# Kernel tuning notes

Hardware: AMD Instinct MI355X
Metric: run time of the kernel (lower is better)

Reference implementation:

```python
import jax, jax.numpy as jnp
import numpy as np

B, T, D, H, L, V = 4, 1024, 1024, 16, 6, 32000
HS = D // H
FF = 4 * D
EPS = 1e-5


def setup_inputs() -> dict:
    key = jax.random.key(0)
    ks = jax.random.split(key, 16)
    s = 0.02
    n = lambda k, shape: (jax.random.normal(k, shape, jnp.float32) * s)
    return {
        'idx': jax.random.randint(ks[0], (B, T), 0, V),
        'targets': jax.random.randint(ks[1], (B, T), 0, V),
        'tok_emb': n(ks[2], (V, D)),
        'pos_emb': n(ks[3], (T, D)),
        'Wq': n(ks[4], (L, D, H, HS)),
        'Wk': n(ks[5], (L, D, H, HS)),
        'Wv': n(ks[6], (L, D, H, HS)),
        'proj_w': n(ks[7], (L, D, D)),
        'proj_b': jnp.zeros((L, D), jnp.float32),
        'ln1_g': jnp.ones((L, D), jnp.float32),
        'ln1_b': jnp.zeros((L, D), jnp.float32),
        'ln2_g': jnp.ones((L, D), jnp.float32),
        'ln2_b': jnp.zeros((L, D), jnp.float32),
        'ff_w1': n(ks[8], (L, D, FF)),
        'ff_b1': jnp.zeros((L, FF), jnp.float32),
        'ff_w2': n(ks[9], (L, FF, D)),
        'ff_b2': jnp.zeros((L, D), jnp.float32),
        'lnf_g': jnp.ones((D,), jnp.float32),
        'lnf_b': jnp.zeros((D,), jnp.float32),
        'head_w': n(ks[10], (D, V)),
        'head_b': jnp.zeros((V,), jnp.float32),
    }


def _ln(x, g, b):
    m = jnp.mean(x, axis=-1, keepdims=True)
    v = jnp.mean((x - m) ** 2, axis=-1, keepdims=True)
    return (x - m) * jax.lax.rsqrt(v + EPS) * g + b


def _forward(idx, targets, tok_emb, pos_emb, Wq, Wk, Wv, proj_w, proj_b,
             ln1_g, ln1_b, ln2_g, ln2_b, ff_w1, ff_b1, ff_w2, ff_b2,
             lnf_g, lnf_b, head_w, head_b):
    b, t = idx.shape
    x = tok_emb[idx] + pos_emb[:t]                       # [B,T,D]
    mask = jnp.tril(jnp.ones((t, t), bool))              # causal
    scale = jnp.float32(D) ** -0.5                       # NOTE: scales by num_dims (c), as in source
    for l in range(L):
        h = _ln(x, ln1_g[l], ln1_b[l])
        q = jnp.einsum('btd,dhs->bhts', h, Wq[l])        # [B,H,T,HS]
        k = jnp.einsum('btd,dhs->bhts', h, Wk[l])
        v = jnp.einsum('btd,dhs->bhts', h, Wv[l])
        w = jnp.einsum('bhts,bhus->bhtu', q, k) * scale  # [B,H,T,T]
        w = jnp.where(mask, w, -jnp.inf)
        w = jax.nn.softmax(w, axis=-1)
        o = jnp.einsum('bhtu,bhus->bhts', w, v)          # [B,H,T,HS]
        o = o.transpose(0, 2, 1, 3).reshape(b, t, D)     # concat heads
        x = x + jnp.einsum('btd,de->bte', o, proj_w[l]) + proj_b[l]
        h2 = _ln(x, ln2_g[l], ln2_b[l])
        ff = jax.nn.relu(jnp.einsum('btd,df->btf', h2, ff_w1[l]) + ff_b1[l])
        x = x + jnp.einsum('btf,fd->btd', ff, ff_w2[l]) + ff_b2[l]
    x = _ln(x, lnf_g, lnf_b)
    logits = jnp.einsum('btd,dv->btv', x, head_w) + head_b
    logits = logits.reshape(b * t, V)
    tgt = targets.reshape(b * t)
    logp = jax.nn.log_softmax(logits, axis=-1)
    loss = -jnp.mean(jnp.take_along_axis(logp, tgt[:, None], axis=-1))
    return logits, loss


def reference(idx, targets, tok_emb, pos_emb, Wq, Wk, Wv, proj_w, proj_b,
              ln1_g, ln1_b, ln2_g, ln2_b, ff_w1, ff_b1, ff_w2, ff_b2,
              lnf_g, lnf_b, head_w, head_b):
    return _forward(idx, targets, tok_emb, pos_emb, Wq, Wk, Wv, proj_w, proj_b,
                    ln1_g, ln1_b, ln2_g, ln2_b, ff_w1, ff_b1, ff_w2, ff_b2,
                    lnf_g, lnf_b, head_w, head_b)
```

## Files before the change

### kernel.cpp

```cpp
#include <hip/hip_runtime.h>

typedef __attribute__((ext_vector_type(8))) short bf16x8;
typedef __attribute__((ext_vector_type(4))) float f32x4;

#define L_LAYERS 6
#define T_SEQ 1024
#define D_MODEL 1024
#define N_HEAD 16
#define HS 64
#define FF_DIM 4096
#define VOCAB 32000
#define BT_ROWS 4096
#define ATTN_SCALE 0.03125f

__device__ __forceinline__ ushort f2bf(float f) {
  unsigned u = __builtin_bit_cast(unsigned, f);
  unsigned r = (u + 0x7fffu + ((u >> 16) & 1u)) >> 16;
  return (ushort)r;
}
__device__ __forceinline__ float waveRedSum(float v) {
#pragma unroll
  for (int off = 32; off; off >>= 1) v += __shfl_xor(v, off);
  return v;
}
__device__ __forceinline__ void gload16(const void* g, void* l) {
  __builtin_amdgcn_global_load_lds(
      (const __attribute__((address_space(1))) unsigned int*)g,
      (__attribute__((address_space(3))) unsigned int*)l, 16, 0, 0);
}

__global__ __launch_bounds__(256) void embed_kernel(const int* __restrict__ idx,
                                                    const float* __restrict__ tok,
                                                    const float* __restrict__ pos,
                                                    float* __restrict__ x) {
  int row = blockIdx.x;
  int tid = threadIdx.x;
  int t = row & (T_SEQ - 1);
  int id = idx[row];
  float4 tv = ((const float4*)(tok + (size_t)id * D_MODEL))[tid];
  float4 pv = ((const float4*)(pos + (size_t)t * D_MODEL))[tid];
  tv.x += pv.x; tv.y += pv.y; tv.z += pv.z; tv.w += pv.w;
  ((float4*)(x + (size_t)row * D_MODEL))[tid] = tv;
}

__global__ __launch_bounds__(256) void ln_kernel(const float* __restrict__ x,
                                                 const float* __restrict__ g,
                                                 const float* __restrict__ b,
                                                 ushort* __restrict__ out) {
  int row = blockIdx.x;
  int tid = threadIdx.x;
  __shared__ float red[4];
  float4 xv = ((const float4*)(x + (size_t)row * D_MODEL))[tid];
  float s = xv.x + xv.y + xv.z + xv.w;
  s = waveRedSum(s);
  if ((tid & 63) == 0) red[tid >> 6] = s;
  __syncthreads();
  float mean = (red[0] + red[1] + red[2] + red[3]) * (1.0f / D_MODEL);
  __syncthreads();
  float d0 = xv.x - mean, d1 = xv.y - mean, d2 = xv.z - mean, d3 = xv.w - mean;
  float v = d0 * d0 + d1 * d1 + d2 * d2 + d3 * d3;
  v = waveRedSum(v);
  if ((tid & 63) == 0) red[tid >> 6] = v;
  __syncthreads();
  float var = (red[0] + red[1] + red[2] + red[3]) * (1.0f / D_MODEL);
  float rstd = rsqrtf(var + 1e-5f);
  float4 gv = ((const float4*)g)[tid];
  float4 bv = ((const float4*)b)[tid];
  ushort4 o;
  o.x = f2bf(d0 * rstd * gv.x + bv.x);
  o.y = f2bf(d1 * rstd * gv.y + bv.y);
  o.z = f2bf(d2 * rstd * gv.z + bv.z);
  o.w = f2bf(d3 * rstd * gv.w + bv.w);
  ((ushort4*)(out + (size_t)row * D_MODEL))[tid] = o;
}

__device__ __forceinline__ void wconv_body(const float* __restrict__ W,
                                           ushort* __restrict__ WT,
                                           int Kd, int Nd, int n0, int k0) {
  __shared__ ushort tile[64][72];
  int tid = threadIdx.x;
#pragma unroll
  for (int i = 0; i < 4; i++) {
    int c = tid + i * 256;
    int row = c >> 4, cc = c & 15;
    float4 wv = *(const float4*)&W[(size_t)(k0 + row) * Nd + n0 + cc * 4];
    tile[row][cc * 4 + 0] = f2bf(wv.x);
    tile[row][cc * 4 + 1] = f2bf(wv.y);
    tile[row][cc * 4 + 2] = f2bf(wv.z);
    tile[row][cc * 4 + 3] = f2bf(wv.w);
  }
  __syncthreads();
#pragma unroll
  for (int i = 0; i < 2; i++) {
    int c = tid + i * 256;
    int n = c >> 3, kc = c & 7;
    __align__(16) ushort tmp[8];
#pragma unroll
    for (int j = 0; j < 8; j++) tmp[j] = tile[kc * 8 + j][n];
    *(int4*)&WT[(size_t)(n0 + n) * Kd + k0 + kc * 8] = *(const int4*)tmp;
  }
}

__global__ __launch_bounds__(256) void wconv_kernel(const float* __restrict__ W,
                                                    ushort* __restrict__ WT,
                                                    int Kd, int Nd) {
  wconv_body(W, WT, Kd, Nd, blockIdx.x * 64, blockIdx.y * 64);
}

__global__ __launch_bounds__(256) void wconv4_kernel(const float* __restrict__ W0,
                                                     const float* __restrict__ W1,
                                                     const float* __restrict__ W2,
                                                     const float* __restrict__ W3,
                                                     ushort* __restrict__ WT,
                                                     int Kd, int Nd) {
  int z = blockIdx.z;
  const float* W = (z == 0) ? W0 : (z == 1) ? W1 : (z == 2) ? W2 : W3;
  wconv_body(W, WT + (size_t)z * Kd * Nd, Kd, Nd, blockIdx.x * 64, blockIdx.y * 64);
}

__global__ __launch_bounds__(256) void vtrans_kernel(const ushort* __restrict__ v,
                                                     ushort* __restrict__ vT) {
  __shared__ ushort tile[64][72];
  int bh = blockIdx.y;
  int t0 = blockIdx.x * 64;
  int tid = threadIdx.x;
#pragma unroll
  for (int i = 0; i < 2; i++) {
    int c = tid + i * 256;
    int row = c >> 3, cc = c & 7;
    *(int4*)&tile[row][cc * 8] =
        *(const int4*)&v[((size_t)bh * T_SEQ + t0 + row) * HS + cc * 8];
  }
  __syncthreads();
#pragma unroll
  for (int i = 0; i < 2; i++) {
    int c = tid + i * 256;
    int hs = c >> 3, tc = c & 7;
    __align__(16) ushort tmp[8];
#pragma unroll
    for (int j = 0; j < 8; j++) tmp[j] = tile[tc * 8 + j][hs];
    *(int4*)&vT[((size_t)bh * HS + hs) * T_SEQ + t0 + tc * 8] = *(const int4*)tmp;
  }
}

template <int BM, int BN, int WM, int WN, int EPI>
__global__ __launch_bounds__(WM * WN * 64, 2) void gemmp_kernel(
    const ushort* __restrict__ A, const ushort* __restrict__ BT, int K,
    const float* __restrict__ bias, float* __restrict__ outf,
    ushort* __restrict__ outb, ushort* __restrict__ outk,
    ushort* __restrict__ outv, int ldo) {
  constexpr int PM = BM / WM, PN = BN / WN;
  constexpr int MR = PM / 16, NR = PN / 16;
  constexpr int ROWS = BM + BN;
  constexpr int NWAVES = WM * WN;
  constexpr int LPW = (ROWS / 8) / NWAVES;
  __shared__ __align__(16) ushort buf[2][ROWS * 64];
  int tid = threadIdx.x;
  int lane = tid & 63, wave = tid >> 6;
  int wm = wave / WN, wn = wave % WN;
  int a = lane & 15, gg = lane >> 4;
  int srow8 = lane >> 3;
  int scol8 = ((lane & 7) ^ (lane >> 3)) * 8;
  int m0 = blockIdx.y * BM, n0 = blockIdx.x * BN;
  f32x4 acc[MR][NR] = {};
  int nt = K >> 6;

  auto STAGE = [&](int t, int d) {
    int k0 = t * 64;
#pragma unroll
    for (int j = 0; j < LPW; j++) {
      int r0 = (wave * LPW + j) * 8;
      if (r0 < BM) {
        gload16(&A[(size_t)(m0 + r0 + srow8) * K + k0 + scol8], &buf[d][r0 * 64]);
      } else {
        gload16(&BT[(size_t)(n0 + (r0 - BM) + srow8) * K + k0 + scol8], &buf[d][r0 * 64]);
      }
    }
  };

  auto COMPUTE = [&](int d) {
    const ushort* bA = &buf[d][0];
    const ushort* bB = &buf[d][BM * 64];
#pragma unroll
    for (int s = 0; s < 2; s++) {
      bf16x8 af[MR], bfr[NR];
#pragma unroll
      for (int i = 0; i < MR; i++) {
        int row = wm * PM + i * 16 + a;
        af[i] = *(const bf16x8*)&bA[row * 64 + (((s * 4 + gg) ^ (a & 7)) * 8)];
      }
#pragma unroll
      for (int j = 0; j < NR; j++) {
        int row = wn * PN + j * 16 + a;
        bfr[j] = *(const bf16x8*)&bB[row * 64 + (((s * 4 + gg) ^ (a & 7)) * 8)];
      }
#pragma unroll
      for (int i = 0; i < MR; i++)
#pragma unroll
        for (int j = 0; j < NR; j++)
          acc[i][j] = __builtin_amdgcn_mfma_f32_16x16x32_bf16(af[i], bfr[j], acc[i][j], 0, 0, 0);
    }
  };

  STAGE(0, 0);
  __syncthreads();
  int cur = 0;
  for (int t = 0; t < nt; t++) {
    if (t + 1 < nt) STAGE(t + 1, cur ^ 1);
    COMPUTE(cur);
    __syncthreads();
    cur ^= 1;
  }

#pragma unroll
  for (int i = 0; i < MR; i++) {
#pragma unroll
    for (int j = 0; j < NR; j++) {
#pragma unroll
      for (int r = 0; r < 4; r++) {
        int mrow = m0 + wm * PM + i * 16 + gg * 4 + r;
        int ncol = n0 + wn * PN + j * 16 + a;
        float v = acc[i][j][r];
        if (EPI == 0) {
          int which = ncol >> 10;
          int n1 = ncol & 1023;
          int h = n1 >> 6, sidx = n1 & 63;
          int bb = mrow >> 10, tt = mrow & 1023;
          ushort* dst = (which == 0) ? outb : (which == 1) ? outk : outv;
          dst[(((size_t)(bb * N_HEAD + h)) * T_SEQ + tt) * HS + sidx] = f2bf(v);
        } else if (EPI == 1) {
          outf[(size_t)mrow * ldo + ncol] += v + bias[ncol];
        } else if (EPI == 2) {
          float t2 = v + bias[ncol];
          outb[(size_t)mrow * ldo + ncol] = f2bf(t2 > 0.0f ? t2 : 0.0f);
        } else {
          outf[(size_t)mrow * ldo + ncol] = v + bias[ncol];
        }
      }
    }
  }
}

template <int EPI>
__global__ __launch_bounds__(512, 2) void gemm8_kernel(
    const ushort* __restrict__ A, const ushort* __restrict__ BT, int K,
    const float* __restrict__ bias, float* __restrict__ outf,
    ushort* __restrict__ outb, int ldo) {
  extern __shared__ __align__(16) ushort lds[];
  int tid = threadIdx.x;
  int lane = tid & 63, wave = tid >> 6;
  int wm = wave >> 1, wn = wave & 1;
  int a = lane & 15, gg = lane >> 4;
  int m0 = blockIdx.y * 256, n0 = blockIdx.x * 256;
  int srow = lane >> 3;
  int scol = ((lane & 7) ^ (lane >> 3)) * 8;
  int nt = K >> 6;
  f32x4 acc[4][8] = {};

  auto stageH = [&](int t, int which) {
    int d = t & 1;
    int k0 = t * 64;
    const ushort* src = (which < 2) ? A : BT;
    int base0 = (which < 2) ? m0 : n0;
    int rh = (which & 1) * 128;
    ushort* dst = lds + ((which < 2) ? 0 : 32768) + d * 16384 + rh * 64;
#pragma unroll
    for (int q = 0; q < 2; q++) {
      int r0 = wave * 16 + q * 8;
      gload16(&src[(size_t)(base0 + rh + r0 + srow) * K + k0 + scol], dst + r0 * 64);
    }
  };

  stageH(0, 0); stageH(0, 1); stageH(0, 2); stageH(0, 3);
  if (nt > 1) { stageH(1, 0); stageH(1, 1); }
  if (nt > 1) asm volatile("s_waitcnt vmcnt(4)" ::: "memory");
  else        asm volatile("s_waitcnt vmcnt(0)" ::: "memory");
  __builtin_amdgcn_s_barrier();

  for (int t = 0; t < nt; t++) {
    int d = t & 1;
    const ushort* bA = lds + d * 16384;
    const ushort* bB = lds + 32768 + d * 16384;
    bf16x8 af[4][2], bf0[4][2];
#pragma unroll
    for (int i = 0; i < 4; i++)
#pragma unroll
      for (int s = 0; s < 2; s++) {
        int row = wm * 64 + i * 16 + a;
        af[i][s] = *(const bf16x8*)&bA[row * 64 + (((s * 4 + gg) ^ (a & 7)) * 8)];
      }
#pragma unroll
    for (int j = 0; j < 4; j++)
#pragma unroll
      for (int s = 0; s < 2; s++) {
        int row = wn * 128 + j * 16 + a;
        bf0[j][s] = *(const bf16x8*)&bB[row * 64 + (((s * 4 + gg) ^ (a & 7)) * 8)];
      }
    if (t + 1 < nt) { stageH(t + 1, 2); stageH(t + 1, 3); }
    __builtin_amdgcn_s_barrier();
    __builtin_amdgcn_sched_barrier(0);
    __builtin_amdgcn_s_setprio(1);
#pragma unroll
    for (int i = 0; i < 4; i++)
#pragma unroll
      for (int j = 0; j < 4; j++)
#pragma unroll
        for (int s = 0; s < 2; s++)
          acc[i][j] = __builtin_amdgcn_mfma_f32_16x16x32_bf16(af[i][s], bf0[j][s], acc[i][j], 0, 0, 0);
    __builtin_amdgcn_s_setprio(0);
    __builtin_amdgcn_sched_barrier(0);
    __builtin_amdgcn_s_barrier();
    bf16x8 bf1[4][2];
#pragma unroll
    for (int j = 0; j < 4; j++)
#pragma unroll
      for (int s = 0; s < 2; s++) {
        int row = wn * 128 + 64 + j * 16 + a;
        bf1[j][s] = *(const bf16x8*)&bB[row * 64 + (((s * 4 + gg) ^ (a & 7)) * 8)];
      }
    if (t + 2 < nt) { stageH(t + 2, 0); stageH(t + 2, 1); }
    __builtin_amdgcn_s_barrier();
    __builtin_amdgcn_sched_barrier(0);
    __builtin_amdgcn_s_setprio(1);
#pragma unroll
    for (int i = 0; i < 4; i++)
#pragma unroll
      for (int j = 0; j < 4; j++)
#pragma unroll
        for (int s = 0; s < 2; s++)
          acc[i][j + 4] = __builtin_amdgcn_mfma_f32_16x16x32_bf16(af[i][s], bf1[j][s], acc[i][j + 4], 0, 0, 0);
    __builtin_amdgcn_s_setprio(0);
    __builtin_amdgcn_sched_barrier(0);
    if (t + 1 < nt) {
      if (t + 2 < nt) asm volatile("s_waitcnt vmcnt(4)" ::: "memory");
      else            asm volatile("s_waitcnt vmcnt(0)" ::: "memory");
    }
    __builtin_amdgcn_s_barrier();
  }

#pragma unroll
  for (int i = 0; i < 4; i++) {
#pragma unroll
    for (int j = 0; j < 8; j++) {
#pragma unroll
      for (int r = 0; r < 4; r++) {
        int mrow = m0 + wm * 64 + i * 16 + gg * 4 + r;
        int ncol = n0 + wn * 128 + j * 16 + a;
        float v = acc[i][j][r];
        if (EPI == 2) {
          float t2 = v + bias[ncol];
          outb[(size_t)mrow * ldo + ncol] = f2bf(t2 > 0.0f ? t2 : 0.0f);
        } else {
          outf[(size_t)mrow * ldo + ncol] = v + bias[ncol];
        }
      }
    }
  }
}

__global__ __launch_bounds__(256) void attn_kernel(const ushort* __restrict__ q,
                                                   const ushort* __restrict__ k,
                                                   const ushort* __restrict__ vT,
                                                   ushort* __restrict__ o) {
  __shared__ __align__(16) ushort Ksm[64 * 72];
  __shared__ __align__(16) ushort Vsm[64 * 72];
  __shared__ __align__(16) ushort Psm[4][16 * 72];
  int tid = threadIdx.x;
  int lane = tid & 63, w = tid >> 6;
  int a = lane & 15, gg = lane >> 4;
  int qt = blockIdx.x, bh = blockIdx.y;
  int qrow_b = qt * 64 + w * 16;
  int qmy = qrow_b + a;

  bf16x8 qf[2];
  const ushort* qbase = q + ((size_t)bh * T_SEQ + qmy) * HS;
  qf[0] = *(const bf16x8*)&qbase[gg * 8];
  qf[1] = *(const bf16x8*)&qbase[32 + gg * 8];

  float m_run = -__builtin_inff();
  float l_run = 0.0f;
  f32x4 oacc[4] = {};
  int nkt = qt + 1;

  for (int kt = 0; kt < nkt; kt++) {
    int k0 = kt * 64;
    __syncthreads();
#pragma unroll
    for (int i = 0; i < 2; i++) {
      int c = tid + i * 256;
      int row = c >> 3, cc = c & 7;
      *(int4*)&Ksm[row * 72 + cc * 8] =
          *(const int4*)&k[((size_t)bh * T_SEQ + k0 + row) * HS + cc * 8];
      *(int4*)&Vsm[row * 72 + cc * 8] =
          *(const int4*)&vT[((size_t)bh * HS + row) * T_SEQ + k0 + cc * 8];
    }
    __syncthreads();

    f32x4 st[4] = {};
#pragma unroll
    for (int ku = 0; ku < 4; ku++) {
#pragma unroll
      for (int s = 0; s < 2; s++) {
        bf16x8 kf = *(const bf16x8*)&Ksm[(ku * 16 + a) * 72 + s * 32 + gg * 8];
        st[ku] = __builtin_amdgcn_mfma_f32_16x16x32_bf16(kf, qf[s], st[ku], 0, 0, 0);
      }
    }

    float pv[16];
    float pm = -__builtin_inff();
#pragma unroll
    for (int ku = 0; ku < 4; ku++) {
#pragma unroll
      for (int r = 0; r < 4; r++) {
        int u = k0 + ku * 16 + gg * 4 + r;
        float val = (u <= qmy) ? st[ku][r] * ATTN_SCALE : -__builtin_inff();
        pv[ku * 4 + r] = val;
        pm = fmaxf(pm, val);
      }
    }
    pm = fmaxf(pm, __shfl_xor(pm, 16));
    pm = fmaxf(pm, __shfl_xor(pm, 32));
    float m_new = fmaxf(m_run, pm);
    float cfac = expf(m_run - m_new);
    float tsum = 0.0f;
#pragma unroll
    for (int xi = 0; xi < 16; xi++) {
      float p = expf(pv[xi] - m_new);
      pv[xi] = p;
      tsum += p;
    }
    tsum += __shfl_xor(tsum, 16);
    tsum += __shfl_xor(tsum, 32);
    l_run = l_run * cfac + tsum;
    m_run = m_new;

    ushort* P = (ushort*)&Psm[w][0];
    asm volatile("s_waitcnt lgkmcnt(0)" ::: "memory");
#pragma unroll
    for (int ku = 0; ku < 4; ku++) {
      ushort4 pw;
      pw.x = f2bf(pv[ku * 4 + 0]);
      pw.y = f2bf(pv[ku * 4 + 1]);
      pw.z = f2bf(pv[ku * 4 + 2]);
      pw.w = f2bf(pv[ku * 4 + 3]);
      *(ushort4*)&P[a * 72 + ku * 16 + gg * 4] = pw;
    }
#pragma unroll
    for (int r = 0; r < 4; r++) {
      float cr = __shfl(cfac, gg * 4 + r);
#pragma unroll
      for (int nb = 0; nb < 4; nb++) oacc[nb][r] *= cr;
    }
    asm volatile("s_waitcnt lgkmcnt(0)" ::: "memory");
#pragma unroll
    for (int kb = 0; kb < 2; kb++) {
      bf16x8 pa = *(const bf16x8*)&P[a * 72 + kb * 32 + gg * 8];
#pragma unroll
      for (int nb = 0; nb < 4; nb++) {
        bf16x8 vb = *(const bf16x8*)&Vsm[(nb * 16 + a) * 72 + kb * 32 + gg * 8];
        oacc[nb] = __builtin_amdgcn_mfma_f32_16x16x32_bf16(pa, vb, oacc[nb], 0, 0, 0);
      }
    }
  }

  float linv = 1.0f / l_run;
  int bb = bh >> 4, hh = bh & 15;
#pragma unroll
  for (int r = 0; r < 4; r++) {
    float li = __shfl(linv, gg * 4 + r);
    int qr = qrow_b + gg * 4 + r;
#pragma unroll
    for (int nb = 0; nb < 4; nb++) {
      o[((size_t)(bb * T_SEQ + qr)) * D_MODEL + hh * HS + nb * 16 + a] =
          f2bf(oacc[nb][r] * li);
    }
  }
}

__global__ __launch_bounds__(256) void loss_row_kernel(const float* __restrict__ logits,
                                                       const int* __restrict__ tgt,
                                                       float* __restrict__ row_loss) {
  int row = blockIdx.x, tid = threadIdx.x;
  __shared__ float redm[4], reds[4];
  const float4* l4 = (const float4*)(logits + (size_t)row * VOCAB);
  float m = -__builtin_inff(), s = 0.0f;
  for (int i = tid; i < VOCAB / 4; i += 256) {
    float4 v = l4[i];
    float cm = fmaxf(fmaxf(v.x, v.y), fmaxf(v.z, v.w));
    if (cm > m) { s *= expf(m - cm); m = cm; }
    s += expf(v.x - m) + expf(v.y - m) + expf(v.z - m) + expf(v.w - m);
  }
#pragma unroll
  for (int off = 32; off; off >>= 1) {
    float om = __shfl_xor(m, off), os = __shfl_xor(s, off);
    float nm = fmaxf(m, om);
    s = s * expf(m - nm) + os * expf(om - nm);
    m = nm;
  }
  if ((tid & 63) == 0) { redm[tid >> 6] = m; reds[tid >> 6] = s; }
  __syncthreads();
  if (tid == 0) {
    float M = fmaxf(fmaxf(redm[0], redm[1]), fmaxf(redm[2], redm[3]));
    float S = reds[0] * expf(redm[0] - M) + reds[1] * expf(redm[1] - M) +
              reds[2] * expf(redm[2] - M) + reds[3] * expf(redm[3] - M);
    row_loss[row] = M + logf(S) - logits[(size_t)row * VOCAB + tgt[row]];
  }
}

__global__ __launch_bounds__(256) void loss_final_kernel(const float* __restrict__ row_loss,
                                                         float* __restrict__ out) {
  int tid = threadIdx.x;
  __shared__ float red[4];
  float s = 0.0f;
  for (int i = tid; i < BT_ROWS; i += 256) s += row_loss[i];
  s = waveRedSum(s);
  if ((tid & 63) == 0) red[tid >> 6] = s;
  __syncthreads();
  if (tid == 0) out[0] = (red[0] + red[1] + red[2] + red[3]) * (1.0f / BT_ROWS);
}

extern "C" void kernel_launch(void* const* d_in, const int* in_sizes, int n_in,
                              void* d_out, int out_size, void* d_ws, size_t ws_size,
                              hipStream_t stream) {
  const int* idx = (const int*)d_in[0];
  const int* tgt = (const int*)d_in[1];
  const float* tok_emb = (const float*)d_in[2];
  const float* pos_emb = (const float*)d_in[3];
  const float* Wq = (const float*)d_in[4];
  const float* Wk = (const float*)d_in[5];
  const float* Wv = (const float*)d_in[6];
  const float* proj_w = (const float*)d_in[7];
  const float* proj_b = (const float*)d_in[8];
  const float* ln1_g = (const float*)d_in[9];
  const float* ln1_b = (const float*)d_in[10];
  const float* ln2_g = (const float*)d_in[11];
  const float* ln2_b = (const float*)d_in[12];
  const float* ff_w1 = (const float*)d_in[13];
  const float* ff_b1 = (const float*)d_in[14];
  const float* ff_w2 = (const float*)d_in[15];
  const float* ff_b2 = (const float*)d_in[16];
  const float* lnf_g = (const float*)d_in[17];
  const float* lnf_b = (const float*)d_in[18];
  const float* head_w = (const float*)d_in[19];
  const float* head_b = (const float*)d_in[20];

  char* ws = (char*)d_ws;
  size_t off = 0;
  float* x = (float*)(ws + off); off += (size_t)BT_ROWS * D_MODEL * 4;
  ushort* h = (ushort*)(ws + off); off += (size_t)BT_ROWS * D_MODEL * 2;
  ushort* qb = (ushort*)(ws + off); off += (size_t)BT_ROWS * D_MODEL * 2;
  ushort* kb = (ushort*)(ws + off); off += (size_t)BT_ROWS * D_MODEL * 2;
  ushort* vb = (ushort*)(ws + off); off += (size_t)BT_ROWS * D_MODEL * 2;
  ushort* vTb = (ushort*)(ws + off); off += (size_t)BT_ROWS * D_MODEL * 2;
  ushort* ob = (ushort*)(ws + off); off += (size_t)BT_ROWS * D_MODEL * 2;
  ushort* ffb = (ushort*)(ws + off); off += (size_t)BT_ROWS * FF_DIM * 2;
  ushort* wqkvT = (ushort*)(ws + off); off += (size_t)4 * D_MODEL * D_MODEL * 2;
  ushort* wprojT = wqkvT + (size_t)3 * D_MODEL * D_MODEL;
  ushort* wff1T = (ushort*)(ws + off); off += (size_t)FF_DIM * D_MODEL * 2;
  ushort* wff2T = (ushort*)(ws + off); off += (size_t)D_MODEL * FF_DIM * 2;
  float* row_loss = (float*)(ws + off); off += (size_t)BT_ROWS * 4;
  ushort* headT = qb;

  float* logits = (float*)d_out;

  embed_kernel<<<BT_ROWS, 256, 0, stream>>>(idx, tok_emb, pos_emb, x);

  for (int l = 0; l < L_LAYERS; l++) {
    size_t wo = (size_t)l * D_MODEL * D_MODEL;
    size_t fo = (size_t)l * D_MODEL * FF_DIM;
    wconv4_kernel<<<dim3(16, 16, 4), 256, 0, stream>>>(Wq + wo, Wk + wo, Wv + wo, proj_w + wo,
                                                       wqkvT, D_MODEL, D_MODEL);
    wconv_kernel<<<dim3(64, 16), 256, 0, stream>>>(ff_w1 + fo, wff1T, D_MODEL, FF_DIM);
    wconv_kernel<<<dim3(16, 64), 256, 0, stream>>>(ff_w2 + fo, wff2T, FF_DIM, D_MODEL);

    ln_kernel<<<BT_ROWS, 256, 0, stream>>>(x, ln1_g + l * D_MODEL, ln1_b + l * D_MODEL, h);
    gemmp_kernel<128, 128, 2, 2, 0><<<dim3(24, 32), 256, 0, stream>>>(
        h, wqkvT, D_MODEL, nullptr, nullptr, qb, kb, vb, 0);
    vtrans_kernel<<<dim3(16, 64), 256, 0, stream>>>(vb, vTb);
    attn_kernel<<<dim3(16, 64), 256, 0, stream>>>(qb, kb, vTb, ob);
    gemmp_kernel<128, 128, 2, 2, 1><<<dim3(8, 32), 256, 0, stream>>>(
        ob, wprojT, D_MODEL, proj_b + l * D_MODEL, x, nullptr, nullptr, nullptr, D_MODEL);
    ln_kernel<<<BT_ROWS, 256, 0, stream>>>(x, ln2_g + l * D_MODEL, ln2_b + l * D_MODEL, h);
    gemm8_kernel<2><<<dim3(16, 16), 512, 131072, stream>>>(
        h, wff1T, D_MODEL, ff_b1 + (size_t)l * FF_DIM, nullptr, ffb, FF_DIM);
    gemmp_kernel<128, 128, 2, 2, 1><<<dim3(8, 32), 256, 0, stream>>>(
        ffb, wff2T, FF_DIM, ff_b2 + l * D_MODEL, x, nullptr, nullptr, nullptr, D_MODEL);
  }

  ln_kernel<<<BT_ROWS, 256, 0, stream>>>(x, lnf_g, lnf_b, h);

  wconv_kernel<<<dim3(500, 16), 256, 0, stream>>>(head_w, headT, D_MODEL, VOCAB);
  gemm8_kernel<3><<<dim3(125, 16), 512, 131072, stream>>>(
      h, headT, D_MODEL, head_b, logits, nullptr, VOCAB);

  loss_row_kernel<<<BT_ROWS, 256, 0, stream>>>(logits, tgt, row_loss);
  loss_final_kernel<<<1, 256, 0, stream>>>(row_loss, logits + (size_t)BT_ROWS * VOCAB);
}
```

Baseline: 2.116 ms.

## Restructure 256x256 GEMM into four-phase pipeline, use it for QKV, swizzle head

Reorganizes the 8-wave 256x256 GEMM so each wave owns a 128x64 sub-tile and each K step runs in four quarter phases. Global staging of the next tiles is interleaved between the MFMA phases, with explicit LDS waits added. Adds a QKV scatter epilogue so the QKV projection moves from the 128x128 kernel onto this larger tile. Adds an XCD-style block-index swizzle for the LM-head GEMM to improve L2 locality. Risks more barriers per iteration and a higher register count.

```diff
diff --git a/kernel.cpp b/kernel.cpp
--- a/kernel.cpp
+++ b/kernel.cpp
@@ -241,113 +241,165 @@
   }
 }
 
-template <int EPI>
+template <int EPI, bool SWZ>
 __global__ __launch_bounds__(512, 2) void gemm8_kernel(
     const ushort* __restrict__ A, const ushort* __restrict__ BT, int K,
     const float* __restrict__ bias, float* __restrict__ outf,
-    ushort* __restrict__ outb, int ldo) {
+    ushort* __restrict__ outb, ushort* __restrict__ outk,
+    ushort* __restrict__ outv, int ldo) {
   extern __shared__ __align__(16) ushort lds[];
   int tid = threadIdx.x;
   int lane = tid & 63, wave = tid >> 6;
-  int wm = wave >> 1, wn = wave & 1;
+  int wm = wave >> 2, wn = wave & 3;
   int a = lane & 15, gg = lane >> 4;
-  int m0 = blockIdx.y * 256, n0 = blockIdx.x * 256;
+  int bx = blockIdx.x, by = blockIdx.y;
+  if (SWZ) {
+    int gx = gridDim.x, nwg = gx * gridDim.y;
+    int wg = by * gx + bx;
+    int id = (wg & 7) * (nwg >> 3) + (wg >> 3);
+    bx = id % gx; by = id / gx;
+  }
+  int m0 = by * 256, n0 = bx * 256;
   int srow = lane >> 3;
   int scol = ((lane & 7) ^ (lane >> 3)) * 8;
   int nt = K >> 6;
-  f32x4 acc[4][8] = {};
-
-  auto stageH = [&](int t, int which) {
+  f32x4 acc[8][4] = {};
+
+  auto stageHalf = [&](int t, int which) {
     int d = t & 1;
     int k0 = t * 64;
     const ushort* src = (which < 2) ? A : BT;
-    int base0 = (which < 2) ? m0 : n0;
-    int rh = (which & 1) * 128;
-    ushort* dst = lds + ((which < 2) ? 0 : 32768) + d * 16384 + rh * 64;
+    int base0 = ((which < 2) ? m0 : n0) + (which & 1) * 128;
+    ushort* dst = lds + ((which < 2) ? 0 : 32768) + d * 16384 + (which & 1) * 8192;
 #pragma unroll
     for (int q = 0; q < 2; q++) {
-      int r0 = wave * 16 + q * 8;
-      gload16(&src[(size_t)(base0 + rh + r0 + srow) * K + k0 + scol], dst + r0 * 64);
+      int r0 = q * 64 + wave * 8;
+      gload16(&src[(size_t)(base0 + r0 + srow) * K + k0 + scol], dst + r0 * 64);
     }
   };
 
-  stageH(0, 0); stageH(0, 1); stageH(0, 2); stageH(0, 3);
-  if (nt > 1) { stageH(1, 0); stageH(1, 1); }
-  if (nt > 1) asm volatile("s_waitcnt vmcnt(4)" ::: "memory");
-  else        asm volatile("s_waitcnt vmcnt(0)" ::: "memory");
+  stageHalf(0, 0); stageHalf(0, 1); stageHalf(0, 2); stageHalf(0, 3);
+  if (nt > 1) {
+    stageHalf(1, 2); stageHalf(1, 3);
+    asm volatile("s_waitcnt vmcnt(4)" ::: "memory");
+  } else {
+    asm volatile("s_waitcnt vmcnt(0)" ::: "memory");
+  }
+  __builtin_amdgcn_sched_barrier(0);
   __builtin_amdgcn_s_barrier();
 
   for (int t = 0; t < nt; t++) {
     int d = t & 1;
     const ushort* bA = lds + d * 16384;
     const ushort* bB = lds + 32768 + d * 16384;
-    bf16x8 af[4][2], bf0[4][2];
+    bf16x8 alo[4][2], ahi[4][2], bj01[2][2], bj23[2][2];
 #pragma unroll
     for (int i = 0; i < 4; i++)
 #pragma unroll
       for (int s = 0; s < 2; s++) {
-        int row = wm * 64 + i * 16 + a;
-        af[i][s] = *(const bf16x8*)&bA[row * 64 + (((s * 4 + gg) ^ (a & 7)) * 8)];
-      }
-#pragma unroll
-    for (int j = 0; j < 4; j++)
+        int row = wm * 128 + i * 16 + a;
+        alo[i][s] = *(const bf16x8*)&bA[row * 64 + (((s * 4 + gg) ^ (a & 7)) * 8)];
+      }
+#pragma unroll
+    for (int j = 0; j < 2; j++)
 #pragma unroll
       for (int s = 0; s < 2; s++) {
-        int row = wn * 128 + j * 16 + a;
-        bf0[j][s] = *(const bf16x8*)&bB[row * 64 + (((s * 4 + gg) ^ (a & 7)) * 8)];
-      }
-    if (t + 1 < nt) { stageH(t + 1, 2); stageH(t + 1, 3); }
-    __builtin_amdgcn_s_barrier();
+        int row = wn * 64 + j * 16 + a;
+        bj01[j][s] = *(const bf16x8*)&bB[row * 64 + (((s * 4 + gg) ^ (a & 7)) * 8)];
+      }
+    if (t + 1 < nt) stageHalf(t + 1, 0);
+    __builtin_amdgcn_s_barrier();
+    asm volatile("s_waitcnt lgkmcnt(0)" ::: "memory");
     __builtin_amdgcn_sched_barrier(0);
     __builtin_amdgcn_s_setprio(1);
 #pragma unroll
     for (int i = 0; i < 4; i++)
 #pragma unroll
-      for (int j = 0; j < 4; j++)
+      for (int j = 0; j < 2; j++)
 #pragma unroll
         for (int s = 0; s < 2; s++)
-          acc[i][j] = __builtin_amdgcn_mfma_f32_16x16x32_bf16(af[i][s], bf0[j][s], acc[i][j], 0, 0, 0);
+          acc[i][j] = __builtin_amdgcn_mfma_f32_16x16x32_bf16(alo[i][s], bj01[j][s], acc[i][j], 0, 0, 0);
     __builtin_amdgcn_s_setprio(0);
-    __builtin_amdgcn_sched_barrier(0);
-    __builtin_amdgcn_s_barrier();
-    bf16x8 bf1[4][2];
-#pragma unroll
-    for (int j = 0; j < 4; j++)
+    __builtin_amdgcn_s_barrier();
+#pragma unroll
+    for (int j = 0; j < 2; j++)
 #pragma unroll
       for (int s = 0; s < 2; s++) {
-        int row = wn * 128 + 64 + j * 16 + a;
-        bf1[j][s] = *(const bf16x8*)&bB[row * 64 + (((s * 4 + gg) ^ (a & 7)) * 8)];
-      }
-    if (t + 2 < nt) { stageH(t + 2, 0); stageH(t + 2, 1); }
-    __builtin_amdgcn_s_barrier();
+        int row = wn * 64 + (j + 2) * 16 + a;
+        bj23[j][s] = *(const bf16x8*)&bB[row * 64 + (((s * 4 + gg) ^ (a & 7)) * 8)];
+      }
+    if (t + 1 < nt) stageHalf(t + 1, 1);
+    __builtin_amdgcn_s_barrier();
+    asm volatile("s_waitcnt lgkmcnt(0)" ::: "memory");
     __builtin_amdgcn_sched_barrier(0);
     __builtin_amdgcn_s_setprio(1);
 #pragma unroll
     for (int i = 0; i < 4; i++)
 #pragma unroll
-      for (int j = 0; j < 4; j++)
+      for (int j = 0; j < 2; j++)
 #pragma unroll
         for (int s = 0; s < 2; s++)
-          acc[i][j + 4] = __builtin_amdgcn_mfma_f32_16x16x32_bf16(af[i][s], bf1[j][s], acc[i][j + 4], 0, 0, 0);
+          acc[i][j + 2] = __builtin_amdgcn_mfma_f32_16x16x32_bf16(alo[i][s], bj23[j][s], acc[i][j + 2], 0, 0, 0);
+    __builtin_amdgcn_s_setprio(0);
+    __builtin_amdgcn_s_barrier();
+#pragma unroll
+    for (int i = 0; i < 4; i++)
+#pragma unroll
+      for (int s = 0; s < 2; s++) {
+        int row = wm * 128 + (i + 4) * 16 + a;
+        ahi[i][s] = *(const bf16x8*)&bA[row * 64 + (((s * 4 + gg) ^ (a & 7)) * 8)];
+      }
+    if (t + 2 < nt) stageHalf(t + 2, 2);
+    __builtin_amdgcn_s_barrier();
+    asm volatile("s_waitcnt lgkmcnt(0)" ::: "memory");
+    __builtin_amdgcn_sched_barrier(0);
+    __builtin_amdgcn_s_setprio(1);
+#pragma unroll
+    for (int i = 0; i < 4; i++)
+#pragma unroll
+      for (int j = 0; j < 2; j++)
+#pragma unroll
+        for (int s = 0; s < 2; s++)
+          acc[i + 4][j] = __builtin_amdgcn_mfma_f32_16x16x32_bf16(ahi[i][s], bj01[j][s], acc[i + 4][j], 0, 0, 0);
+    __builtin_amdgcn_s_setprio(0);
+    __builtin_amdgcn_s_barrier();
+    if (t + 2 < nt) stageHalf(t + 2, 3);
+    __builtin_amdgcn_s_barrier();
+    __builtin_amdgcn_s_setprio(1);
+#pragma unroll
+    for (int i = 0; i < 4; i++)
+#pragma unroll
+      for (int j = 0; j < 2; j++)
+#pragma unroll
+        for (int s = 0; s < 2; s++)
+          acc[i + 4][j + 2] = __builtin_amdgcn_mfma_f32_16x16x32_bf16(ahi[i][s], bj23[j][s], acc[i + 4][j + 2], 0, 0, 0);
     __builtin_amdgcn_s_setprio(0);
     __builtin_amdgcn_sched_barrier(0);
     if (t + 1 < nt) {
       if (t + 2 < nt) asm volatile("s_waitcnt vmcnt(4)" ::: "memory");
       else            asm volatile("s_waitcnt vmcnt(0)" ::: "memory");
-    }
-    __builtin_amdgcn_s_barrier();
-  }
-
-#pragma unroll
-  for (int i = 0; i < 4; i++) {
-#pragma unroll
-    for (int j = 0; j < 8; j++) {
+      __builtin_amdgcn_sched_barrier(0);
+    }
+    __builtin_amdgcn_s_barrier();
+  }
+
+#pragma unroll
+  for (int i = 0; i < 8; i++) {
+#pragma unroll
+    for (int j = 0; j < 4; j++) {
 #pragma unroll
       for (int r = 0; r < 4; r++) {
-        int mrow = m0 + wm * 64 + i * 16 + gg * 4 + r;
-        int ncol = n0 + wn * 128 + j * 16 + a;
+        int mrow = m0 + wm * 128 + i * 16 + gg * 4 + r;
+        int ncol = n0 + wn * 64 + j * 16 + a;
         float v = acc[i][j][r];
-        if (EPI == 2) {
+        if (EPI == 0) {
+          int which = ncol >> 10;
+          int n1 = ncol & 1023;
+          int h = n1 >> 6, sidx = n1 & 63;
+          int bb = mrow >> 10, tt = mrow & 1023;
+          ushort* dst = (which == 0) ? outb : (which == 1) ? outk : outv;
+          dst[(((size_t)(bb * N_HEAD + h)) * T_SEQ + tt) * HS + sidx] = f2bf(v);
+        } else if (EPI == 2) {
           float t2 = v + bias[ncol];
           outb[(size_t)mrow * ldo + ncol] = f2bf(t2 > 0.0f ? t2 : 0.0f);
         } else {
@@ -574,15 +626,15 @@
     wconv_kernel<<<dim3(16, 64), 256, 0, stream>>>(ff_w2 + fo, wff2T, FF_DIM, D_MODEL);
 
     ln_kernel<<<BT_ROWS, 256, 0, stream>>>(x, ln1_g + l * D_MODEL, ln1_b + l * D_MODEL, h);
-    gemmp_kernel<128, 128, 2, 2, 0><<<dim3(24, 32), 256, 0, stream>>>(
+    gemm8_kernel<0, false><<<dim3(12, 16), 512, 131072, stream>>>(
         h, wqkvT, D_MODEL, nullptr, nullptr, qb, kb, vb, 0);
     vtrans_kernel<<<dim3(16, 64), 256, 0, stream>>>(vb, vTb);
     attn_kernel<<<dim3(16, 64), 256, 0, stream>>>(qb, kb, vTb, ob);
     gemmp_kernel<128, 128, 2, 2, 1><<<dim3(8, 32), 256, 0, stream>>>(
         ob, wprojT, D_MODEL, proj_b + l * D_MODEL, x, nullptr, nullptr, nullptr, D_MODEL);
     ln_kernel<<<BT_ROWS, 256, 0, stream>>>(x, ln2_g + l * D_MODEL, ln2_b + l * D_MODEL, h);
-    gemm8_kernel<2><<<dim3(16, 16), 512, 131072, stream>>>(
-        h, wff1T, D_MODEL, ff_b1 + (size_t)l * FF_DIM, nullptr, ffb, FF_DIM);
+    gemm8_kernel<2, false><<<dim3(16, 16), 512, 131072, stream>>>(
+        h, wff1T, D_MODEL, ff_b1 + (size_t)l * FF_DIM, nullptr, ffb, nullptr, nullptr, FF_DIM);
     gemmp_kernel<128, 128, 2, 2, 1><<<dim3(8, 32), 256, 0, stream>>>(
         ffb, wff2T, FF_DIM, ff_b2 + l * D_MODEL, x, nullptr, nullptr, nullptr, D_MODEL);
   }
@@ -590,8 +642,8 @@
   ln_kernel<<<BT_ROWS, 256, 0, stream>>>(x, lnf_g, lnf_b, h);
 
   wconv_kernel<<<dim3(500, 16), 256, 0, stream>>>(head_w, headT, D_MODEL, VOCAB);
-  gemm8_kernel<3><<<dim3(125, 16), 512, 131072, stream>>>(
-      h, headT, D_MODEL, head_b, logits, nullptr, VOCAB);
+  gemm8_kernel<3, true><<<dim3(125, 16), 512, 131072, stream>>>(
+      h, headT, D_MODEL, head_b, logits, nullptr, nullptr, nullptr, VOCAB);
 
   loss_row_kernel<<<BT_ROWS, 256, 0, stream>>>(logits, tgt, row_loss);
   loss_final_kernel<<<1, 256, 0, stream>>>(row_loss, logits + (size_t)BT_ROWS * VOCAB);
```

Result: faster. 2.067 ms (-2.3%).
